# Performance work log

Hardware: AMD Instinct MI355X
Metric: run time of the kernel (lower is better)

## Reference

```python
import jax, jax.numpy as jnp
import numpy as np

B, S, H, R = 4, 4096, 768, 242
HK = H // 3  # k/v/attn-output feature dim (256)
THETA = 10000.0


def _rope_table(seq_len, dim, theta=THETA):
    # Reproduces LlamaRotaryEmbedding.forward: returns [seq_len, dim] = cat(sin, cos)
    pos = jnp.arange(seq_len, dtype=jnp.float32)
    freqs = theta ** (-jnp.arange(0, dim, 2, dtype=jnp.float32) / dim)  # [dim/2]
    ang = pos[:, None] * freqs[None, :]  # [S, dim/2]
    return jnp.concatenate([jnp.sin(ang), jnp.cos(ang)], axis=-1)  # [S, dim]


def setup_inputs() -> dict:
    key = jax.random.key(0)
    ks = jax.random.split(key, 9)
    init = lambda k, shape: (jax.random.normal(k, shape, dtype=jnp.float32) * 0.02)
    return {
        "x": jax.random.normal(ks[0], (B, S, H), dtype=jnp.float32),
        # torch nn.Linear weights have shape [out_features, in_features]; y = x @ W.T
        "q_low": init(ks[1], (R, H)),  "q_high": init(ks[2], (H, R)),
        "k_low": init(ks[3], (R, H)),  "k_high": init(ks[4], (HK, R)),
        "v_low": init(ks[5], (R, H)),  "v_high": init(ks[6], (HK, R)),
        "o_low": init(ks[7], (R, HK)), "o_high": init(ks[8], (H, R)),
    }


def reference(x, q_low, q_high, k_low, k_high, v_low, v_high, o_low, o_high):
    b, s, h = x.shape
    # NOTE: in the original module, rope_emb(q) / rope_emb(k) discard the projected
    # q/k values and return the same [S, H] sin/cos position table, so q_proj/k_proj
    # are dead code (XLA will DCE them). We keep only the live computation.
    v = (x @ v_low.T) @ v_high.T  # [B, S, HK] factorized v projection
    t = _rope_table(s, h)         # q = k = t, shape [S, H]
    attn = jax.nn.softmax(t @ t.T, axis=-1)  # [S, S], input-independent
    ctx = jnp.einsum('st,btd->bsd', attn, v)  # [B, S, HK]
    return (ctx @ o_low.T) @ o_high.T         # [B, S, H]
```

## Files before the change

### kernel.cpp

```cpp
#include <hip/hip_runtime.h>
#include <hip/hip_bf16.h>


typedef __bf16 bf16x8 __attribute__((ext_vector_type(8)));
typedef float  f32x4  __attribute__((ext_vector_type(4)));

#define GLD16(g, l) __builtin_amdgcn_global_load_lds(                         \
    (const __attribute__((address_space(1))) void*)(g),                       \
    (__attribute__((address_space(3))) void*)(l), 16, 0, 0)


__global__ __launch_bounds__(256) void prep_ptvlt(const float* __restrict__ vh,
                                                  const float* __restrict__ ol,
                                                  const float* __restrict__ vl,
                                                  float* __restrict__ pt,
                                                  __bf16* __restrict__ vlt) {
    if (blockIdx.x < 242) {
        int j = blockIdx.x, i = threadIdx.x;
        float s = 0.f;
        if (i < 242) {
            for (int k = 0; k < 256; ++k)
                s += vh[k * 242 + i] * ol[j * 256 + k];
        }
        pt[j * 256 + i] = s;
    } else {
        int n = (blockIdx.x - 242) * 256 + threadIdx.x;
        int i = n >> 8, r = n & 255;
        vlt[n] = (r < 242) ? (__bf16)vl[r * 768 + i] : (__bf16)0.f;
    }
}

__global__ __launch_bounds__(256) void prep_q(const float* __restrict__ pt,
                                              const float* __restrict__ oh,
                                              __bf16* __restrict__ qb) {
    int j = blockIdx.x, r = threadIdx.x;
    float s = 0.f;
    for (int k = 0; k < 242; ++k)
        s += pt[k * 256 + r] * oh[j * 242 + k];
    qb[j * 256 + r] = (__bf16)s;
}

__global__ __launch_bounds__(256, 2) void gemm_nt_w(const __bf16* __restrict__ A,
                                                    const __bf16* __restrict__ Bt,
                                                    __bf16* __restrict__ C,
                                                    int Ndim, int Kdim) {
    __shared__ alignas(16) __bf16 lA[128 * 32];
    __shared__ alignas(16) __bf16 lB[128 * 32];

    const int tid  = threadIdx.x;
    const int wave = tid >> 6, lane = tid & 63;
    const int quad = lane >> 4, l16 = lane & 15;
    const int wm = (wave >> 1) * 64, wn = (wave & 1) * 64;

    const __bf16* Ab = A + (long)blockIdx.x * 128 * Kdim;
    const __bf16* Bb = Bt + (long)blockIdx.y * 128 * Kdim;

    f32x4 acc[4][4] = {};

    for (int k0 = 0; k0 < Kdim; k0 += 32) {
#pragma unroll
        for (int it = 0; it < 2; ++it) {
            int cb = it * 256 + wave * 64;
            int c  = cb + lane;
            GLD16(Ab + (long)(c >> 2) * Kdim + k0 + (c & 3) * 8, &lA[cb * 8]);
            GLD16(Bb + (long)(c >> 2) * Kdim + k0 + (c & 3) * 8, &lB[cb * 8]);
        }
        __syncthreads();

        bf16x8 af[4], bfr[4];
#pragma unroll
        for (int i = 0; i < 4; ++i)
            af[i] = *(const bf16x8*)&lA[(wm + i * 16 + l16) * 32 + quad * 8];
#pragma unroll
        for (int i = 0; i < 4; ++i)
            bfr[i] = *(const bf16x8*)&lB[(wn + i * 16 + l16) * 32 + quad * 8];

#pragma unroll
        for (int mi = 0; mi < 4; ++mi)
#pragma unroll
            for (int ni = 0; ni < 4; ++ni)
                acc[mi][ni] = __builtin_amdgcn_mfma_f32_16x16x32_bf16(
                    af[mi], bfr[ni], acc[mi][ni], 0, 0, 0);

        __syncthreads();
    }

    const long rbase = (long)blockIdx.x * 128 + wm + quad * 4;
    const long cbase = (long)blockIdx.y * 128 + wn + l16;
#pragma unroll
    for (int mi = 0; mi < 4; ++mi)
#pragma unroll
        for (int ni = 0; ni < 4; ++ni)
#pragma unroll
            for (int j = 0; j < 4; ++j)
                C[(rbase + mi * 16 + j) * Ndim + cbase + ni * 16] =
                    (__bf16)acc[mi][ni][j];
}

__global__ __launch_bounds__(256, 4) void gemm_xw(const float* __restrict__ A,
                                                  const __bf16* __restrict__ Bt,
                                                  float* __restrict__ C) {
    __shared__ alignas(16) __bf16 lA[2][64 * 32];
    __shared__ alignas(16) __bf16 lB[2][128 * 32];

    const int tid  = threadIdx.x;
    const int wave = tid >> 6, lane = tid & 63;
    const int quad = lane >> 4, l16 = lane & 15;
    const int wm = (wave >> 1) * 32, wn = (wave & 1) * 64;

    const int id   = blockIdx.x;
    const int xcd  = id & 7;
    const int slot = id >> 3;
    const int nt   = slot % 6;
    const int mt   = xcd + 8 * (slot / 6);

    const float*  Ab = A  + (long)mt * 64 * 768;
    const __bf16* Bb = Bt + (long)nt * 128 * 768;

    const float* ga = Ab + (tid >> 2) * 768 + (tid & 3) * 8;

    f32x4 pa0 = *(const f32x4*)(ga), pa1 = *(const f32x4*)(ga + 4);
#pragma unroll
    for (int it = 0; it < 2; ++it) {
        int cb = it * 256 + wave * 64;
        int c  = cb + lane;
        GLD16(Bb + (long)(c >> 2) * 768 + (c & 3) * 8, &lB[0][cb * 8]);
    }
    {
        bf16x8 h0 = { (__bf16)pa0[0], (__bf16)pa0[1], (__bf16)pa0[2], (__bf16)pa0[3],
                      (__bf16)pa1[0], (__bf16)pa1[1], (__bf16)pa1[2], (__bf16)pa1[3] };
        *(bf16x8*)&lA[0][tid * 8] = h0;
    }
    __syncthreads();

    f32x4 acc[2][4] = {};

    for (int k = 0; k < 24; ++k) {
        const int cur = k & 1, nxt = cur ^ 1;
        const int koff = (k + 1) * 32;

        bf16x8 af[2], bfr[4];
#pragma unroll
        for (int i = 0; i < 2; ++i)
            af[i] = *(const bf16x8*)&lA[cur][(wm + i * 16 + l16) * 32 + quad * 8];
#pragma unroll
        for (int i = 0; i < 4; ++i)
            bfr[i] = *(const bf16x8*)&lB[cur][(wn + i * 16 + l16) * 32 + quad * 8];

        if (k < 23) {
#pragma unroll
            for (int it = 0; it < 2; ++it) {
                int cb = it * 256 + wave * 64;
                int c  = cb + lane;
                GLD16(Bb + (long)(c >> 2) * 768 + koff + (c & 3) * 8,
                      &lB[nxt][cb * 8]);
            }
            pa0 = *(const f32x4*)(ga + koff);
            pa1 = *(const f32x4*)(ga + koff + 4);
        }

#pragma unroll
        for (int mi = 0; mi < 2; ++mi)
#pragma unroll
            for (int ni = 0; ni < 4; ++ni)
                acc[mi][ni] = __builtin_amdgcn_mfma_f32_16x16x32_bf16(
                    af[mi], bfr[ni], acc[mi][ni], 0, 0, 0);

        if (k < 23) {
            bf16x8 h0 = { (__bf16)pa0[0], (__bf16)pa0[1], (__bf16)pa0[2], (__bf16)pa0[3],
                          (__bf16)pa1[0], (__bf16)pa1[1], (__bf16)pa1[2], (__bf16)pa1[3] };
            *(bf16x8*)&lA[nxt][tid * 8] = h0;
            __syncthreads();
        }
    }

    const long rbase = (long)mt * 64 + wm + quad * 4;
    const long cbase = (long)nt * 128 + wn + l16;
#pragma unroll
    for (int mi = 0; mi < 2; ++mi)
#pragma unroll
        for (int ni = 0; ni < 4; ++ni)
#pragma unroll
            for (int j = 0; j < 4; ++j)
                C[(rbase + mi * 16 + j) * 768 + cbase + ni * 16] = acc[mi][ni][j];
}


extern "C" void kernel_launch(void* const* d_in, const int* in_sizes, int n_in,
                              void* d_out, int out_size, void* d_ws, size_t ws_size,
                              hipStream_t stream) {
    const float* x      = (const float*)d_in[0];
    const float* v_low  = (const float*)d_in[5];
    const float* v_high = (const float*)d_in[6];
    const float* o_low  = (const float*)d_in[7];
    const float* o_high = (const float*)d_in[8];
    float* out = (float*)d_out;

    char* ws = (char*)d_ws;
    float*  pt  = (float*) (ws + 0);
    __bf16* qb  = (__bf16*)(ws + 262144);
    __bf16* vlt = (__bf16*)(ws + 655360);
    __bf16* wtb = (__bf16*)(ws + 1048576);

    prep_ptvlt<<<1010, 256, 0, stream>>>(v_high, o_low, v_low, pt, vlt);
    prep_q    <<<768,  256, 0, stream>>>(pt, o_high, qb);

    gemm_nt_w<<<dim3(6, 6), 256, 0, stream>>>(qb, vlt, wtb, 768, 256);

    gemm_xw<<<1536, 256, 0, stream>>>(x, wtb, out);
}
```

Measured before the change: 175.0 us.

## Restructure x·W GEMM so each block computes full 768-column row strip

The final GEMM now launches one 512-thread block per 64-row tile of x and covers all 768 output columns, so each x tile is read from global memory and converted to bf16 only once instead of six times. Weight fragments are loaded straight from global memory into registers and double-buffered there, with no LDS staging. The A tile in LDS is padded to a stride of 72 to reduce bank conflicts. In exchange there are far fewer blocks (256), much higher register pressure (96 accumulator registers plus 48 for the B buffers), and the weight matrix is re-read by every block through the caches.

```diff
diff --git a/kernel.cpp b/kernel.cpp
--- a/kernel.cpp
+++ b/kernel.cpp
@@ -97,92 +97,94 @@
                     (__bf16)acc[mi][ni][j];
 }
 
-__global__ __launch_bounds__(256, 4) void gemm_xw(const float* __restrict__ A,
+__global__ __launch_bounds__(512, 2) void gemm_xw(const float* __restrict__ A,
                                                   const __bf16* __restrict__ Bt,
                                                   float* __restrict__ C) {
-    __shared__ alignas(16) __bf16 lA[2][64 * 32];
-    __shared__ alignas(16) __bf16 lB[2][128 * 32];
+    __shared__ __bf16 lA[2][64 * 72];
 
     const int tid  = threadIdx.x;
     const int wave = tid >> 6, lane = tid & 63;
     const int quad = lane >> 4, l16 = lane & 15;
-    const int wm = (wave >> 1) * 32, wn = (wave & 1) * 64;
-
-    const int id   = blockIdx.x;
-    const int xcd  = id & 7;
-    const int slot = id >> 3;
-    const int nt   = slot % 6;
-    const int mt   = xcd + 8 * (slot / 6);
-
-    const float*  Ab = A  + (long)mt * 64 * 768;
-    const __bf16* Bb = Bt + (long)nt * 128 * 768;
-
-    const float* ga = Ab + (tid >> 2) * 768 + (tid & 3) * 8;
-
-    f32x4 pa0 = *(const f32x4*)(ga), pa1 = *(const f32x4*)(ga + 4);
-#pragma unroll
-    for (int it = 0; it < 2; ++it) {
-        int cb = it * 256 + wave * 64;
-        int c  = cb + lane;
-        GLD16(Bb + (long)(c >> 2) * 768 + (c & 3) * 8, &lB[0][cb * 8]);
-    }
+
+    const int mt = blockIdx.x;
+    const float* Ab = A + (long)mt * 64 * 768;
+
+    const int srow = tid >> 3, scol = (tid & 7) * 8;
+    const float* ga = Ab + srow * 768 + scol;
+
+    const int nb = wave * 96;
+    const __bf16* Bw = Bt + (long)(nb + l16) * 768 + quad * 8;
+
+    f32x4 acc[6][4] = {};
+    bf16x8 bcur[6][2], bnxt[6][2];
+
+    f32x4 a0 = *(const f32x4*)(ga);
+    f32x4 a1 = *(const f32x4*)(ga + 4);
+#pragma unroll
+    for (int g = 0; g < 6; ++g)
+#pragma unroll
+        for (int kf = 0; kf < 2; ++kf)
+            bcur[g][kf] = *(const bf16x8*)(Bw + (long)g * 16 * 768 + kf * 32);
     {
-        bf16x8 h0 = { (__bf16)pa0[0], (__bf16)pa0[1], (__bf16)pa0[2], (__bf16)pa0[3],
-                      (__bf16)pa1[0], (__bf16)pa1[1], (__bf16)pa1[2], (__bf16)pa1[3] };
-        *(bf16x8*)&lA[0][tid * 8] = h0;
+        bf16x8 h = { (__bf16)a0[0], (__bf16)a0[1], (__bf16)a0[2], (__bf16)a0[3],
+                     (__bf16)a1[0], (__bf16)a1[1], (__bf16)a1[2], (__bf16)a1[3] };
+        *(bf16x8*)&lA[0][srow * 72 + scol] = h;
     }
     __syncthreads();
 
-    f32x4 acc[2][4] = {};
-
-    for (int k = 0; k < 24; ++k) {
-        const int cur = k & 1, nxt = cur ^ 1;
-        const int koff = (k + 1) * 32;
-
-        bf16x8 af[2], bfr[4];
-#pragma unroll
-        for (int i = 0; i < 2; ++i)
-            af[i] = *(const bf16x8*)&lA[cur][(wm + i * 16 + l16) * 32 + quad * 8];
-#pragma unroll
-        for (int i = 0; i < 4; ++i)
-            bfr[i] = *(const bf16x8*)&lB[cur][(wn + i * 16 + l16) * 32 + quad * 8];
-
-        if (k < 23) {
-#pragma unroll
-            for (int it = 0; it < 2; ++it) {
-                int cb = it * 256 + wave * 64;
-                int c  = cb + lane;
-                GLD16(Bb + (long)(c >> 2) * 768 + koff + (c & 3) * 8,
-                      &lB[nxt][cb * 8]);
-            }
-            pa0 = *(const f32x4*)(ga + koff);
-            pa1 = *(const f32x4*)(ga + koff + 4);
-        }
-
-#pragma unroll
-        for (int mi = 0; mi < 2; ++mi)
-#pragma unroll
-            for (int ni = 0; ni < 4; ++ni)
-                acc[mi][ni] = __builtin_amdgcn_mfma_f32_16x16x32_bf16(
-                    af[mi], bfr[ni], acc[mi][ni], 0, 0, 0);
-
-        if (k < 23) {
-            bf16x8 h0 = { (__bf16)pa0[0], (__bf16)pa0[1], (__bf16)pa0[2], (__bf16)pa0[3],
-                          (__bf16)pa1[0], (__bf16)pa1[1], (__bf16)pa1[2], (__bf16)pa1[3] };
-            *(bf16x8*)&lA[nxt][tid * 8] = h0;
+#pragma unroll
+    for (int c = 0; c < 12; ++c) {
+        const int cur = c & 1, nxt = cur ^ 1;
+        const int koff = (c + 1) * 64;
+
+        if (c < 11) {
+            a0 = *(const f32x4*)(ga + koff);
+            a1 = *(const f32x4*)(ga + koff + 4);
+#pragma unroll
+            for (int g = 0; g < 6; ++g)
+#pragma unroll
+                for (int kf = 0; kf < 2; ++kf)
+                    bnxt[g][kf] = *(const bf16x8*)(Bw + (long)g * 16 * 768 +
+                                                   koff + kf * 32);
+        }
+
+#pragma unroll
+        for (int kf = 0; kf < 2; ++kf) {
+            bf16x8 af[4];
+#pragma unroll
+            for (int m = 0; m < 4; ++m)
+                af[m] = *(const bf16x8*)
+                        &lA[cur][(m * 16 + l16) * 72 + kf * 32 + quad * 8];
+#pragma unroll
+            for (int g = 0; g < 6; ++g)
+#pragma unroll
+                for (int m = 0; m < 4; ++m)
+                    acc[g][m] = __builtin_amdgcn_mfma_f32_16x16x32_bf16(
+                        af[m], bcur[g][kf], acc[g][m], 0, 0, 0);
+        }
+
+        if (c < 11) {
+            bf16x8 h = { (__bf16)a0[0], (__bf16)a0[1], (__bf16)a0[2], (__bf16)a0[3],
+                         (__bf16)a1[0], (__bf16)a1[1], (__bf16)a1[2], (__bf16)a1[3] };
+            *(bf16x8*)&lA[nxt][srow * 72 + scol] = h;
+#pragma unroll
+            for (int g = 0; g < 6; ++g)
+#pragma unroll
+                for (int kf = 0; kf < 2; ++kf)
+                    bcur[g][kf] = bnxt[g][kf];
             __syncthreads();
         }
     }
 
-    const long rbase = (long)mt * 64 + wm + quad * 4;
-    const long cbase = (long)nt * 128 + wn + l16;
-#pragma unroll
-    for (int mi = 0; mi < 2; ++mi)
-#pragma unroll
-        for (int ni = 0; ni < 4; ++ni)
+    const long rb = (long)mt * 64 + quad * 4;
+    const int  cb = nb + l16;
+#pragma unroll
+    for (int g = 0; g < 6; ++g)
+#pragma unroll
+        for (int m = 0; m < 4; ++m)
 #pragma unroll
             for (int j = 0; j < 4; ++j)
-                C[(rbase + mi * 16 + j) * 768 + cbase + ni * 16] = acc[mi][ni][j];
+                C[(rb + m * 16 + j) * 768 + cb + g * 16] = acc[g][m][j];
 }
 
 
@@ -207,5 +209,5 @@
 
     gemm_nt_w<<<dim3(6, 6), 256, 0, stream>>>(qb, vlt, wtb, 768, 256);
 
-    gemm_xw<<<1536, 256, 0, stream>>>(x, wtb, out);
-}
+    gemm_xw<<<256, 512, 0, stream>>>(x, wtb, out);
+}
```

Result: faster. 171.0 us (-2.3%).
